# Kernel optimization log

Hardware: AMD Instinct MI355X
Metric: run time of the kernel (lower is better)

The kernel has to match this reference:

```python
import jax, jax.numpy as jnp
import numpy as np

B, T, D, C = 16, 4096, 1024, 128


def setup_inputs() -> dict:
    key = jax.random.key(0)
    ks = jax.random.split(key, 15)

    def w(k, out_dim, in_dim):
        return jax.random.normal(k, (out_dim, in_dim), jnp.float32) / np.sqrt(in_dim).astype(np.float32)

    return {
        "x": jax.random.normal(ks[0], (B, T, D), jnp.float32),
        "Wq": w(ks[1], C, D), "bq": jnp.zeros((C,), jnp.float32),
        "Wk": w(ks[2], C, D), "bk": jnp.zeros((C,), jnp.float32),
        "Wv": w(ks[3], C, D), "bv": jnp.zeros((C,), jnp.float32),
        "Wa": w(ks[4], 1, D), "ba": jnp.zeros((1,), jnp.float32),
        "Wb": w(ks[5], 1, D), "bb": jnp.zeros((1,), jnp.float32),
        "Wg": w(ks[6], C, D), "bg": jnp.zeros((C,), jnp.float32),
        "Wo": w(ks[7], D, C), "bo": jnp.zeros((D,), jnp.float32),
    }


def reference(x, Wq, bq, Wk, bk, Wv, bv, Wa, ba, Wb, bb, Wg, bg, Wo, bo):
    # Projections (torch Linear: y = x @ W.T + b)
    q = x @ Wq.T + bq                                   # (B,T,C)
    k = x @ Wk.T + bk
    k = k / jnp.maximum(jnp.linalg.norm(k, axis=-1, keepdims=True), 1e-12)  # F.normalize
    v = x @ Wv.T + bv
    alpha = jax.nn.sigmoid(x @ Wa.T + ba)               # (B,T,1)
    beta = jax.nn.sigmoid(x @ Wb.T + bb)                # (B,T,1)
    gate = jax.nn.sigmoid(x @ Wg.T + bg)                # (B,T,C)

    Bb, Tt, Dd = x.shape
    Cc = q.shape[-1]

    def step(S, inp):
        q_t, k_t, v_t, a_t, b_t = inp                   # (B,C),(B,C),(B,C),(B,1),(B,1)
        a = a_t[:, :, None]                              # (B,1,1)
        b = b_t[:, :, None]                              # (B,1,1)
        # S @ (a*(I - b*k k^T)) = a*(S - b*(S k) k^T)
        Sk = jnp.einsum('bij,bj->bi', S, k_t)            # (B,C)
        S = a * (S - b * (Sk[:, :, None] * k_t[:, None, :])) \
            + b * (v_t[:, :, None] * k_t[:, None, :])
        o = jnp.einsum('bi,bij->bj', q_t, S)             # (B,C)
        return S, o

    xs = (q.swapaxes(0, 1), k.swapaxes(0, 1), v.swapaxes(0, 1),
          alpha.swapaxes(0, 1), beta.swapaxes(0, 1))     # time-major
    S0 = jnp.zeros((Bb, Cc, Cc), x.dtype)
    _, o = jax.lax.scan(step, S0, xs)                    # o: (T,B,C)
    o = o.swapaxes(0, 1) * gate                          # (B,T,C)
    return o @ Wo.T + bo                                 # (B,T,D)
```

## Files before the change

kernel.cpp:

```cpp
#include <hip/hip_runtime.h>
#include <hip/hip_bf16.h>
#include <math.h>

#define NB 16
#define NT 4096
#define ND 1024
#define NCC 128
#define LCH 64
#define NCHUNK 64
#define BTROWS 65536

typedef __bf16 v8bf __attribute__((ext_vector_type(8)));
typedef float  v4f  __attribute__((ext_vector_type(4)));

static __device__ __forceinline__ float sig_(float x){ return 1.0f/(1.0f + __expf(-x)); }
static __device__ __forceinline__ float dot4_(float4 a, float4 b){
    return a.x*b.x + a.y*b.y + a.z*b.z + a.w*b.w;
}

static __device__ __forceinline__ v8bf pack8(float4 a, float4 b){
    v8bf v;
    v[0]=(__bf16)a.x; v[1]=(__bf16)a.y; v[2]=(__bf16)a.z; v[3]=(__bf16)a.w;
    v[4]=(__bf16)b.x; v[5]=(__bf16)b.y; v[6]=(__bf16)b.z; v[7]=(__bf16)b.w;
    return v;
}

static __device__ __forceinline__ void gload16(const void* g, void* l){
    __builtin_amdgcn_global_load_lds(
        (const __attribute__((address_space(1))) unsigned int*)g,
        (__attribute__((address_space(3))) unsigned int*)l, 16, 0, 0);
}

__global__ __launch_bounds__(256) void k_xcast(
    const float* __restrict__ x, const float* __restrict__ Wa,
    const float* __restrict__ Wb, const float* __restrict__ ba,
    const float* __restrict__ bb2, __bf16* __restrict__ xbf,
    float* __restrict__ ab, float* __restrict__ beb)
{
    const int tid = threadIdx.x;
    const int w = tid >> 6, lane = tid & 63;
    const size_t row = (size_t)blockIdx.x*4 + w;
    const float* xr = x + row*ND + lane*16;
    float4 f0 = ((const float4*)xr)[0];
    float4 f1 = ((const float4*)xr)[1];
    float4 f2 = ((const float4*)xr)[2];
    float4 f3 = ((const float4*)xr)[3];
    const float4* wa = (const float4*)(Wa + lane*16);
    const float4* wb = (const float4*)(Wb + lane*16);
    float da = dot4_(f0,wa[0]) + dot4_(f1,wa[1]) + dot4_(f2,wa[2]) + dot4_(f3,wa[3]);
    float db = dot4_(f0,wb[0]) + dot4_(f1,wb[1]) + dot4_(f2,wb[2]) + dot4_(f3,wb[3]);
    __bf16* xd = xbf + row*ND + lane*16;
    *(v8bf*)(xd)   = pack8(f0,f1);
    *(v8bf*)(xd+8) = pack8(f2,f3);
    #pragma unroll
    for (int m=1;m<64;m<<=1){ da += __shfl_xor(da,m,64); db += __shfl_xor(db,m,64); }
    if (lane == 0){
        ab[row]  = sig_(da + ba[0]);
        beb[row] = sig_(db + bb2[0]);
    }
}

__global__ __launch_bounds__(256) void k_wcast(
    const float* __restrict__ Wq, const float* __restrict__ Wk,
    const float* __restrict__ Wv, const float* __restrict__ Wg,
    __bf16* __restrict__ wbf)
{
    const int tid = threadIdx.x;
    const int w = tid >> 6, lane = tid & 63;
    const int row = blockIdx.x*4 + w;
    const float* src = (row < 128) ? Wq + (size_t)row*ND
                     : (row < 256) ? Wk + (size_t)(row-128)*ND
                     : (row < 384) ? Wv + (size_t)(row-256)*ND
                     :               Wg + (size_t)(row-384)*ND;
    const float4* s4 = (const float4*)(src + lane*16);
    float4 f0=s4[0], f1=s4[1], f2=s4[2], f3=s4[3];
    __bf16* xd = wbf + (size_t)row*ND + lane*16;
    *(v8bf*)(xd)   = pack8(f0,f1);
    *(v8bf*)(xd+8) = pack8(f2,f3);
}

__global__ __launch_bounds__(256) void k_proj2(
    const __bf16* __restrict__ xbf, const __bf16* __restrict__ wbf,
    const float* __restrict__ bq, const float* __restrict__ bk,
    const float* __restrict__ bv, const float* __restrict__ bg,
    float* __restrict__ qb, float* __restrict__ kb2,
    float* __restrict__ vb, float* __restrict__ gb)
{
    __shared__ __attribute__((aligned(16))) __bf16 As[128*64];
    __shared__ __attribute__((aligned(16))) __bf16 Bs[128*64];
    const int tid = threadIdx.x;
    const int lane = tid & 63, w = tid >> 6;
    const int q4 = lane >> 4, l16 = lane & 15;
    const int wm = w >> 1, wn = w & 1;

    const int f = blockIdx.x;
    const int xcd = f & 7, j = f >> 3;
    const int m0 = ((xcd << 6) + (j >> 2)) * 128;
    const int n0 = (j & 3) * 128;

    v4f acc[4][4] = {};

    for (int k0 = 0; k0 < ND; k0 += 64){
        __syncthreads();
        #pragma unroll
        for (int i=0;i<4;i++){
            const int r  = (w*4+i)*8 + (lane >> 3);
            const int ce = (((lane & 7) ^ (r & 7)) << 3);
            gload16(xbf + (size_t)(m0 + r)*ND + k0 + ce, (char*)As + (w*4+i)*1024);
            gload16(wbf + (size_t)(n0 + r)*ND + k0 + ce, (char*)Bs + (w*4+i)*1024);
        }
        __syncthreads();
        #pragma unroll
        for (int ks=0; ks<2; ks++){
            v8bf af[4], bf[4];
            #pragma unroll
            for (int mf=0; mf<4; mf++){
                const int r = wm*64 + mf*16 + l16;
                af[mf] = *(const v8bf*)((const char*)As + r*128 + (((ks*4+q4) ^ (r&7)) << 4));
            }
            #pragma unroll
            for (int nf=0; nf<4; nf++){
                const int r = wn*64 + nf*16 + l16;
                bf[nf] = *(const v8bf*)((const char*)Bs + r*128 + (((ks*4+q4) ^ (r&7)) << 4));
            }
            #pragma unroll
            for (int mf=0; mf<4; mf++)
                #pragma unroll
                for (int nf=0; nf<4; nf++)
                    acc[mf][nf] = __builtin_amdgcn_mfma_f32_16x16x32_bf16(af[mf], bf[nf], acc[mf][nf], 0,0,0);
        }
    }

    #pragma unroll
    for (int mf=0; mf<4; mf++){
        #pragma unroll
        for (int nf=0; nf<4; nf++){
            const int ng  = n0 + wn*64 + nf*16 + l16;
            const int col = ng & 127;
            const int sel = ng >> 7;
            const float bias = (sel==0) ? bq[col] : (sel==1) ? bk[col]
                             : (sel==2) ? bv[col] : bg[col];
            #pragma unroll
            for (int r2=0;r2<4;r2++){
                const int m = m0 + wm*64 + mf*16 + q4*4 + r2;
                const float val = acc[mf][nf][r2] + bias;
                const size_t off = (size_t)m*NCC + col;
                if      (sel == 0) qb[off]  = val;
                else if (sel == 1) kb2[off] = val;
                else if (sel == 2) vb[off]  = val;
                else               gb[off]  = sig_(val);
            }
        }
    }
}

__global__ __launch_bounds__(256) void k_knorm(float* __restrict__ kb){
    const int tid = threadIdx.x;
    const int w = tid >> 6, lane = tid & 63;
    const size_t row = (size_t)blockIdx.x*4 + w;
    float* kr = kb + row*NCC;
    float a = kr[lane], b = kr[lane+64];
    float ss = a*a + b*b;
    #pragma unroll
    for (int m=1;m<64;m<<=1) ss += __shfl_xor(ss, m, 64);
    float inv = 1.0f / fmaxf(sqrtf(ss), 1e-12f);
    kr[lane] = a*inv; kr[lane+64] = b*inv;
}

#define KSWZ(t, j)   ((t)*132 + ((((((j)>>2) ^ ((t)&7))) << 2) | ((j)&3)))
#define KSWZ4(t, j4) ((t)*132 + ((((j4) ^ ((t)&7))) << 2))
#define TSWZ(row, g) ((row)*72 + ((((g) ^ ((row)&7))) << 3))

#define SOLVE_LOOP(RHS_EXPR) \
    _Pragma("unroll") \
    for (int t=0;t<64;t++){ \
        const float* Gr = &Gsh[t*68]; \
        float s0=0.f,s1=0.f,s2=0.f,s3=0.f; \
        _Pragma("unroll") \
        for (int s4=0; s4+4<=t; s4+=4){ \
            float4 g = *(const float4*)(Gr+s4); \
            s0 += g.x*u[s4]; s1 += g.y*u[s4+1]; s2 += g.z*u[s4+2]; s3 += g.w*u[s4+3]; \
        } \
        _Pragma("unroll") \
        for (int s=(t & ~3); s<t; s++) s0 += Gr[s]*u[s]; \
        u[t] = bsh[t]*((RHS_EXPR) - ((s0+s1)+(s2+s3))); \
    }

__global__ __launch_bounds__(256) void k_phaseA(
    const float* __restrict__ kb, float* __restrict__ vb, __bf16* __restrict__ Mb,
    const float* __restrict__ ab, const float* __restrict__ beb,
    float* __restrict__ lgb, __bf16* __restrict__ PTb, float* __restrict__ Rb)
{
    __shared__ __attribute__((aligned(16))) float Ksh[LCH*132];
    __shared__ __attribute__((aligned(16))) float Vsh[LCH*132];
    __shared__ __attribute__((aligned(16))) float Gsh[LCH*68];
    __shared__ __attribute__((aligned(16))) __bf16 KT [NCC*72];
    __shared__ __attribute__((aligned(16))) __bf16 EUT[NCC*72];
    __shared__ __attribute__((aligned(16))) __bf16 EMT[NCC*72];
    __shared__ float lgs[LCH], bsh[LCH], esh[LCH], gam[LCH];

    const int tid = threadIdx.x;
    const int b = blockIdx.x >> 6;
    const int c = blockIdx.x & 63;
    const size_t base = (size_t)b*NT + (size_t)c*LCH;

    if (tid < LCH){
        float la = __logf(fmaxf(ab[base+tid], 1e-30f));
        float ps = la;
        #pragma unroll
        for (int off=1; off<64; off<<=1){
            float o = __shfl_up(ps, off, 64);
            if ((tid & 63) >= off) ps += o;
        }
        lgs[tid] = ps;
        bsh[tid] = beb[base+tid];
    }
    {
        const int row = tid >> 2, seg = tid & 3;
        const float* ks = kb + (base+row)*NCC + seg*32;
        const float* vs = vb + (base+row)*NCC + seg*32;
        #pragma unroll
        for (int i=0;i<32;i+=4){
            float4 kv = *(const float4*)(ks+i);
            float4 vv = *(const float4*)(vs+i);
            *(float4*)(&Ksh[KSWZ4(row, ((seg*32+i)>>2))]) = kv;
            *(float4*)(&Vsh[row*132 + seg*32 + i]) = vv;
        }
    }
    __syncthreads();
    if (tid < LCH){
        lgb[base+tid] = lgs[tid];
        esh[tid] = __expf(lgs[LCH-1] - lgs[tid]);
        gam[tid] = __expf(lgs[tid]);
    }
    for (int idx = tid; idx < (LCH*(LCH+1))/2; idx += 256){
        int t = (int)((sqrtf(8.f*(float)idx + 1.f) - 1.f)*0.5f);
        while ((t+1)*(t+2)/2 <= idx) t++;
        while (t*(t+1)/2 > idx) t--;
        const int s = idx - (t*(t+1))/2;
        float dot = 0.f;
        #pragma unroll 8
        for (int j4=0;j4<32;j4++){
            float4 u = *(const float4*)(&Ksh[KSWZ4(s,j4)]);
            float4 v = *(const float4*)(&Ksh[KSWZ4(t,j4)]);
            dot += u.x*v.x + u.y*v.y + u.z*v.z + u.w*v.w;
        }
        Gsh[t*68+s] = __expf(lgs[t]-lgs[s])*dot;
    }
    {
        const int j = tid & 127, th = tid >> 7;
        #pragma unroll
        for (int g=0; g<4; g++){
            const int t0 = th*32 + g*8;
            v8bf pk;
            #pragma unroll
            for (int e=0;e<8;e++) pk[e] = (__bf16)Ksh[KSWZ(t0+e, j)];
            *(v8bf*)(&KT[TSWZ(j, (t0>>3))]) = pk;
        }
    }
    __syncthreads();

    {
        const int half = tid >> 7, cix = tid & 127;
        float u[64];
        if (half == 0){
            SOLVE_LOOP(Vsh[t*132 + cix])
            #pragma unroll
            for (int t=0;t<64;t++) vb[(base+t)*NCC + cix] = u[t];
            #pragma unroll
            for (int g=0; g<8; g++){
                v8bf pk;
                #pragma unroll
                for (int e=0;e<8;e++) pk[e] = (__bf16)(esh[g*8+e]*u[g*8+e]);
                *(v8bf*)(&EUT[TSWZ(cix, g)]) = pk;
            }
        } else {
            SOLVE_LOOP(gam[t]*Ksh[KSWZ(t, cix)])
            #pragma unroll
            for (int t=0;t<64;t++) Mb[(base+t)*NCC + cix] = (__bf16)u[t];
            #pragma unroll
            for (int g=0; g<8; g++){
                v8bf pk;
                #pragma unroll
                for (int e=0;e<8;e++) pk[e] = (__bf16)(esh[g*8+e]*u[g*8+e]);
                *(v8bf*)(&EMT[TSWZ(cix, g)]) = pk;
            }
        }
    }
    __syncthreads();

    {
        const int lane = tid & 63, w = tid >> 6;
        const int q4 = lane >> 4, l16 = lane & 15;
        const int wm = w >> 1, wn = w & 1;
        const float gl = gam[LCH-1];
        const size_t pbase = ((size_t)(b*NCHUNK + c))*NCC*NCC;
        {
            v4f pacc[4][4] = {};
            #pragma unroll
            for (int ks=0; ks<2; ks++){
                v8bf af[4], bf[4];
                #pragma unroll
                for (int mf=0; mf<4; mf++)
                    af[mf] = *(const v8bf*)(&KT[TSWZ(wm*64+mf*16+l16, ks*4+q4)]);
                #pragma unroll
                for (int nf=0; nf<4; nf++)
                    bf[nf] = *(const v8bf*)(&EMT[TSWZ(wn*64+nf*16+l16, ks*4+q4)]);
                #pragma unroll
                for (int mf=0; mf<4; mf++)
                    #pragma unroll
                    for (int nf=0; nf<4; nf++)
                        pacc[mf][nf] = __builtin_amdgcn_mfma_f32_16x16x32_bf16(af[mf], bf[nf], pacc[mf][nf], 0,0,0);
            }
            #pragma unroll
            for (int mf=0; mf<4; mf++){
                #pragma unroll
                for (int nf=0; nf<4; nf++){
                    const int m = wn*64 + nf*16 + l16;
                    #pragma unroll
                    for (int r=0;r<4;r++){
                        const int j = wm*64 + mf*16 + q4*4 + r;
                        float v = -pacc[mf][nf][r];
                        if (j == m) v += gl;
                        PTb[pbase + (size_t)j*NCC + m] = (__bf16)v;
                    }
                }
            }
        }
        {
            v4f racc[4][4] = {};
            #pragma unroll
            for (int ks=0; ks<2; ks++){
                v8bf af[4], bf[4];
                #pragma unroll
                for (int mf=0; mf<4; mf++)
                    af[mf] = *(const v8bf*)(&EUT[TSWZ(wm*64+mf*16+l16, ks*4+q4)]);
                #pragma unroll
                for (int nf=0; nf<4; nf++)
                    bf[nf] = *(const v8bf*)(&KT[TSWZ(wn*64+nf*16+l16, ks*4+q4)]);
                #pragma unroll
                for (int mf=0; mf<4; mf++)
                    #pragma unroll
                    for (int nf=0; nf<4; nf++)
                        racc[mf][nf] = __builtin_amdgcn_mfma_f32_16x16x32_bf16(af[mf], bf[nf], racc[mf][nf], 0,0,0);
            }
            #pragma unroll
            for (int mf=0; mf<4; mf++){
                #pragma unroll
                for (int nf=0; nf<4; nf++){
                    const int jj = wn*64 + nf*16 + l16;
                    #pragma unroll
                    for (int r=0;r<4;r++){
                        const int i = wm*64 + mf*16 + q4*4 + r;
                        Rb[pbase + (size_t)i*NCC + jj] = racc[mf][nf][r];
                    }
                }
            }
        }
    }
}

__global__ __launch_bounds__(256) void k_phaseB(
    const __bf16* __restrict__ PTb, const float* __restrict__ Rb, float* __restrict__ Sb)
{
    __shared__ __attribute__((aligned(16))) float Ssh[16*132];
    const int tid = threadIdx.x;
    const int b = blockIdx.x >> 3, rb = blockIdx.x & 7;
    const int r0 = rb*16;
    const int lane = tid & 63, w = tid >> 6;
    const int q4 = lane >> 4, l16 = lane & 15;
    for (int i=tid; i<16*132; i+=256) Ssh[i] = 0.f;
    __syncthreads();
    for (int c=0; c<NCHUNK; c++){
        const size_t pbase = ((size_t)(b*NCHUNK + c))*NCC*NCC;
        {
            const int row = tid >> 4, cg = (tid & 15)*8;
            float* dst = Sb + pbase + (size_t)(r0+row)*NCC + cg;
            *(float4*)(dst)   = *(const float4*)(&Ssh[row*132+cg]);
            *(float4*)(dst+4) = *(const float4*)(&Ssh[row*132+cg+4]);
        }
        if (c == NCHUNK-1) break;
        v8bf af[4];
        #pragma unroll
        for (int ks=0; ks<4; ks++){
            const float* sr = &Ssh[l16*132 + ks*32 + q4*8];
            v8bf t;
            #pragma unroll
            for (int j=0;j<8;j++) t[j] = (__bf16)sr[j];
            af[ks] = t;
        }
        __syncthreads();
        v4f acc[2] = {};
        #pragma unroll
        for (int nt=0; nt<2; nt++){
            const int n0 = w*32 + nt*16;
            #pragma unroll
            for (int ks=0; ks<4; ks++){
                v8bf bf = *(const v8bf*)(PTb + pbase + (size_t)(n0+l16)*NCC + ks*32 + q4*8);
                acc[nt] = __builtin_amdgcn_mfma_f32_16x16x32_bf16(af[ks], bf, acc[nt], 0,0,0);
            }
        }
        #pragma unroll
        for (int nt=0; nt<2; nt++){
            const int n = w*32 + nt*16 + l16;
            #pragma unroll
            for (int r=0;r<4;r++){
                const int rowl = q4*4 + r;
                Ssh[rowl*132 + n] = acc[nt][r] + Rb[pbase + (size_t)(r0+rowl)*NCC + n];
            }
        }
        __syncthreads();
    }
}

__global__ __launch_bounds__(256) void k_phaseC(
    const float* __restrict__ qb, const float* __restrict__ kb,
    const float* __restrict__ Ub, const __bf16* __restrict__ Mb,
    const float* __restrict__ Sb, const float* __restrict__ lgb,
    float* __restrict__ gb)
{
    __shared__ __attribute__((aligned(16))) float S0T[NCC*132];
    __shared__ __attribute__((aligned(16))) __bf16 Msh[LCH*136];
    __shared__ __attribute__((aligned(16))) __bf16 Qsh[LCH*136];
    __shared__ __attribute__((aligned(16))) __bf16 Ksh[LCH*136];
    __shared__ __attribute__((aligned(16))) __bf16 Wsh[LCH*136];
    __shared__ __attribute__((aligned(16))) float Ash[LCH*68];
    __shared__ float lgs[LCH];

    const int tid = threadIdx.x;
    const int b = blockIdx.x >> 6, c = blockIdx.x & 63;
    const size_t base = (size_t)b*NT + (size_t)c*LCH;
    const size_t pbase = ((size_t)(b*NCHUNK + c))*NCC*NCC;

    {
        const int i = tid >> 1, j0 = (tid & 1)*64;
        const float* src = Sb + pbase + (size_t)i*NCC + j0;
        #pragma unroll 4
        for (int j=0;j<64;j+=4){
            float4 v = *(const float4*)(src+j);
            S0T[(j0+j  )*132 + i] = v.x;
            S0T[(j0+j+1)*132 + i] = v.y;
            S0T[(j0+j+2)*132 + i] = v.z;
            S0T[(j0+j+3)*132 + i] = v.w;
        }
    }
    {
        const int row = tid >> 2, seg = tid & 3;
        const __bf16* ms = Mb + (base+row)*NCC + seg*32;
        const float* qs = qb + (base+row)*NCC + seg*32;
        const float* ks = kb + (base+row)*NCC + seg*32;
        *(v8bf*)(&Msh[row*136+seg*32])    = *(const v8bf*)(ms);
        *(v8bf*)(&Msh[row*136+seg*32+8])  = *(const v8bf*)(ms+8);
        *(v8bf*)(&Msh[row*136+seg*32+16]) = *(const v8bf*)(ms+16);
        *(v8bf*)(&Msh[row*136+seg*32+24]) = *(const v8bf*)(ms+24);
        #pragma unroll 8
        for (int i=0;i<32;i++){
            Qsh[row*136+seg*32+i] = (__bf16)qs[i];
            Ksh[row*136+seg*32+i] = (__bf16)ks[i];
        }
    }
    if (tid < LCH) lgs[tid] = lgb[base+tid];
    __syncthreads();

    {
        const int tg = tid >> 5, ig = tid & 31;
        float acc[8][4] = {};
        for (int j=0;j<NCC;j++){
            float m8[8];
            #pragma unroll
            for (int r=0;r<8;r++) m8[r] = (float)Msh[(tg*8+r)*136 + j];
            float4 sv = *(const float4*)(&S0T[j*132 + ig*4]);
            #pragma unroll
            for (int r=0;r<8;r++){
                acc[r][0] += m8[r]*sv.x; acc[r][1] += m8[r]*sv.y;
                acc[r][2] += m8[r]*sv.z; acc[r][3] += m8[r]*sv.w;
            }
        }
        #pragma unroll
        for (int r=0;r<8;r++){
            const int t = tg*8+r;
            const float4 uv = *(const float4*)(Ub + (base+t)*NCC + ig*4);
            Wsh[t*136+ig*4+0] = (__bf16)(uv.x - acc[r][0]);
            Wsh[t*136+ig*4+1] = (__bf16)(uv.y - acc[r][1]);
            Wsh[t*136+ig*4+2] = (__bf16)(uv.z - acc[r][2]);
            Wsh[t*136+ig*4+3] = (__bf16)(uv.w - acc[r][3]);
        }
    }
    float o2[8][4];
    {
        const int tg = tid >> 5, jg = tid & 31;
        float acc[8][4] = {};
        for (int i=0;i<NCC;i++){
            float q8[8];
            #pragma unroll
            for (int r=0;r<8;r++) q8[r] = (float)Qsh[(tg*8+r)*136 + i];
            float s4[4];
            #pragma unroll
            for (int rr=0;rr<4;rr++) s4[rr] = S0T[(jg+32*rr)*132 + i];
            #pragma unroll
            for (int r=0;r<8;r++){
                acc[r][0] += q8[r]*s4[0]; acc[r][1] += q8[r]*s4[1];
                acc[r][2] += q8[r]*s4[2]; acc[r][3] += q8[r]*s4[3];
            }
        }
        #pragma unroll
        for (int r=0;r<8;r++){
            const float g = __expf(lgs[tg*8+r]);
            #pragma unroll
            for (int d=0;d<4;d++) o2[r][d] = g*acc[r][d];
        }
    }
    __syncthreads();
    {
        const int tg2 = tid >> 4, sg = tid & 15;
        float acc[4][4] = {};
        for (int i=0;i<NCC;i++){
            float qv[4], wv[4];
            #pragma unroll
            for (int r=0;r<4;r++){
                qv[r] = (float)Qsh[(tg2+16*r)*136 + i];
                wv[r] = (float)Wsh[(sg+16*r)*136 + i];
            }
            #pragma unroll
            for (int a2=0;a2<4;a2++){
                acc[a2][0] += qv[a2]*wv[0]; acc[a2][1] += qv[a2]*wv[1];
                acc[a2][2] += qv[a2]*wv[2]; acc[a2][3] += qv[a2]*wv[3];
            }
        }
        #pragma unroll
        for (int a2=0;a2<4;a2++){
            const int t = tg2 + 16*a2;
            #pragma unroll
            for (int b2=0;b2<4;b2++){
                const int s = sg + 16*b2;
                Ash[t*68+s] = (s <= t) ? __expf(lgs[t]-lgs[s])*acc[a2][b2] : 0.f;
            }
        }
    }
    __syncthreads();
    {
        const int tg = tid >> 5, jg = tid & 31;
        float acc[8][4] = {};
        for (int s=0;s<LCH;s++){
            float a8[8];
            #pragma unroll
            for (int r=0;r<8;r++) a8[r] = Ash[(tg*8+r)*68 + s];
            float k4[4];
            #pragma unroll
            for (int rr=0;rr<4;rr++) k4[rr] = (float)Ksh[s*136 + jg + 32*rr];
            #pragma unroll
            for (int r=0;r<8;r++){
                acc[r][0] += a8[r]*k4[0]; acc[r][1] += a8[r]*k4[1];
                acc[r][2] += a8[r]*k4[2]; acc[r][3] += a8[r]*k4[3];
            }
        }
        #pragma unroll
        for (int r=0;r<8;r++){
            const int t = tg*8+r;
            #pragma unroll
            for (int d=0;d<4;d++){
                const int j = jg + 32*d;
                const size_t off = (base+t)*NCC + j;
                gb[off] = (acc[r][d] + o2[r][d]) * gb[off];
            }
        }
    }
}

__global__ __launch_bounds__(256) void k_out(
    const float* __restrict__ ob, const float* __restrict__ Wo,
    const float* __restrict__ bo, float* __restrict__ out)
{
    __shared__ __attribute__((aligned(16))) __bf16 As[128*40];
    __shared__ __attribute__((aligned(16))) __bf16 Bs[64*40];
    const int tid = threadIdx.x;
    const int m0 = blockIdx.x*128, n0 = blockIdx.y*64;
    const int lane = tid & 63, w = tid >> 6;
    const int q4 = lane >> 4, l16 = lane & 15;
    const int arow = tid >> 1, aseg = tid & 1;
    const int brow = tid >> 2, bseg = tid & 3;
    const float* asrc = ob + (size_t)(m0+arow)*NCC;
    const float* bsrc = Wo + (size_t)(n0+brow)*NCC;

    v4f acc[2][4] = {};

    for (int k0=0; k0<NCC; k0+=32){
        __syncthreads();
        {
            float4 f0 = *(const float4*)(asrc + k0 + aseg*16);
            float4 f1 = *(const float4*)(asrc + k0 + aseg*16 + 4);
            float4 f2 = *(const float4*)(asrc + k0 + aseg*16 + 8);
            float4 f3 = *(const float4*)(asrc + k0 + aseg*16 + 12);
            *(v8bf*)(&As[arow*40 + aseg*16])     = pack8(f0,f1);
            *(v8bf*)(&As[arow*40 + aseg*16 + 8]) = pack8(f2,f3);
        }
        {
            float4 g0 = *(const float4*)(bsrc + k0 + bseg*8);
            float4 g1 = *(const float4*)(bsrc + k0 + bseg*8 + 4);
            *(v8bf*)(&Bs[brow*40 + bseg*8]) = pack8(g0,g1);
        }
        __syncthreads();
        v8bf af0 = *(const v8bf*)(&As[(w*32 + l16)*40 + q4*8]);
        v8bf af1 = *(const v8bf*)(&As[(w*32 + 16 + l16)*40 + q4*8]);
        #pragma unroll
        for (int nt=0; nt<4; nt++){
            v8bf bf = *(const v8bf*)(&Bs[(nt*16 + l16)*40 + q4*8]);
            acc[0][nt] = __builtin_amdgcn_mfma_f32_16x16x32_bf16(af0, bf, acc[0][nt], 0,0,0);
            acc[1][nt] = __builtin_amdgcn_mfma_f32_16x16x32_bf16(af1, bf, acc[1][nt], 0,0,0);
        }
    }
    #pragma unroll
    for (int mt=0; mt<2; mt++){
        #pragma unroll
        for (int nt=0; nt<4; nt++){
            const int n = n0 + nt*16 + l16;
            const float bias = bo[n];
            #pragma unroll
            for (int r=0;r<4;r++){
                const int m = m0 + w*32 + mt*16 + q4*4 + r;
                out[(size_t)m*ND + n] = acc[mt][nt][r] + bias;
            }
        }
    }
}

extern "C" void kernel_launch(void* const* d_in, const int* in_sizes, int n_in,
                              void* d_out, int out_size, void* d_ws, size_t ws_size,
                              hipStream_t stream)
{
    const float* x  = (const float*)d_in[0];
    const float* Wq = (const float*)d_in[1];
    const float* bq = (const float*)d_in[2];
    const float* Wk = (const float*)d_in[3];
    const float* bk = (const float*)d_in[4];
    const float* Wv = (const float*)d_in[5];
    const float* bv = (const float*)d_in[6];
    const float* Wa = (const float*)d_in[7];
    const float* ba = (const float*)d_in[8];
    const float* Wb = (const float*)d_in[9];
    const float* bb2= (const float*)d_in[10];
    const float* Wg = (const float*)d_in[11];
    const float* bg = (const float*)d_in[12];
    const float* Wo = (const float*)d_in[13];
    const float* bo = (const float*)d_in[14];

    char* ws = (char*)d_ws;
    const size_t SZ = (size_t)BTROWS*NCC*4;
    float*  qb  = (float*)(ws + 0*SZ);
    float*  kb  = (float*)(ws + 1*SZ);
    float*  vb  = (float*)(ws + 2*SZ);
    __bf16* Mb  = (__bf16*)(ws + 3*SZ);
    float*  gb  = (float*)(ws + 4*SZ);
    float*  Sb  = (float*)(ws + 5*SZ);
    float*  Rb  = (float*)(ws + 7*SZ);
    __bf16* PTb = (__bf16*)(ws + 9*SZ);
    float*  ab  = (float*)(ws + 10*SZ);
    float*  beb = (float*)(ws + 10*SZ + 262144);
    float*  lgb = (float*)(ws + 10*SZ + 524288);
    __bf16* xbf = (__bf16*)(ws + 5*SZ);
    __bf16* wbf = (__bf16*)(ws + 9*SZ);
    if (ws_size < 10*SZ + 786432) return;

    dim3 blk(256);
    k_wcast <<<dim3(128),            blk, 0, stream>>>(Wq,Wk,Wv,Wg,wbf);
    k_xcast <<<dim3(BTROWS/4),       blk, 0, stream>>>(x,Wa,Wb,ba,bb2,xbf,ab,beb);
    k_proj2 <<<dim3(2048),           blk, 0, stream>>>(xbf,wbf,bq,bk,bv,bg,qb,kb,vb,gb);
    k_knorm <<<dim3(BTROWS/4),       blk, 0, stream>>>(kb);
    k_phaseA<<<dim3(NB*NCHUNK),      blk, 0, stream>>>(kb, vb, Mb, ab, beb, lgb, PTb, Rb);
    k_phaseB<<<dim3(NB*8),           blk, 0, stream>>>(PTb, Rb, Sb);
    k_phaseC<<<dim3(NB*NCHUNK),      blk, 0, stream>>>(qb, kb, vb, Mb, Sb, lgb, gb);
    k_out   <<<dim3(BTROWS/128, 16), blk, 0, stream>>>(gb, Wo, bo, (float*)d_out);
}
```

Baseline: 1.208 ms.

## Rewrite chunk output phase with bf16 MFMA and swizzled LDS layouts

Replaces the four scalar FP32 FMA matmuls in k_phaseC (M·S0, Q·S0, Q·Wᵀ, A·K) with 16x16x32 bf16 MFMA instructions. S0 is staged into LDS in bf16 in both row and transposed forms, K is stored transposed with an XOR swizzle (TSWZ), and the MA buffer is reused for the decay-masked attention matrix. This targets the ALU-bound scalar loops and cuts LDS footprint. It adds more bf16 rounding of S0 and the intermediate attention matrix, and the kernel relies on a TSWZ macro defined outside the shown hunk.

```diff
diff --git a/kernel.cpp b/kernel.cpp
--- a/kernel.cpp
+++ b/kernel.cpp
@@ -419,149 +419,142 @@
     const float* __restrict__ Sb, const float* __restrict__ lgb,
     float* __restrict__ gb)
 {
-    __shared__ __attribute__((aligned(16))) float S0T[NCC*132];
-    __shared__ __attribute__((aligned(16))) __bf16 Msh[LCH*136];
-    __shared__ __attribute__((aligned(16))) __bf16 Qsh[LCH*136];
-    __shared__ __attribute__((aligned(16))) __bf16 Ksh[LCH*136];
+    __shared__ __attribute__((aligned(16))) __bf16 S0r[NCC*136];
+    __shared__ __attribute__((aligned(16))) __bf16 S0t[NCC*136];
+    __shared__ __attribute__((aligned(16))) __bf16 MA [LCH*136];
     __shared__ __attribute__((aligned(16))) __bf16 Wsh[LCH*136];
-    __shared__ __attribute__((aligned(16))) float Ash[LCH*68];
+    __shared__ __attribute__((aligned(16))) __bf16 KT [NCC*72];
     __shared__ float lgs[LCH];
 
     const int tid = threadIdx.x;
     const int b = blockIdx.x >> 6, c = blockIdx.x & 63;
     const size_t base = (size_t)b*NT + (size_t)c*LCH;
     const size_t pbase = ((size_t)(b*NCHUNK + c))*NCC*NCC;
-
-    {
-        const int i = tid >> 1, j0 = (tid & 1)*64;
-        const float* src = Sb + pbase + (size_t)i*NCC + j0;
-        #pragma unroll 4
-        for (int j=0;j<64;j+=4){
-            float4 v = *(const float4*)(src+j);
-            S0T[(j0+j  )*132 + i] = v.x;
-            S0T[(j0+j+1)*132 + i] = v.y;
-            S0T[(j0+j+2)*132 + i] = v.z;
-            S0T[(j0+j+3)*132 + i] = v.w;
-        }
-    }
-    {
-        const int row = tid >> 2, seg = tid & 3;
-        const __bf16* ms = Mb + (base+row)*NCC + seg*32;
-        const float* qs = qb + (base+row)*NCC + seg*32;
-        const float* ks = kb + (base+row)*NCC + seg*32;
-        *(v8bf*)(&Msh[row*136+seg*32])    = *(const v8bf*)(ms);
-        *(v8bf*)(&Msh[row*136+seg*32+8])  = *(const v8bf*)(ms+8);
-        *(v8bf*)(&Msh[row*136+seg*32+16]) = *(const v8bf*)(ms+16);
-        *(v8bf*)(&Msh[row*136+seg*32+24]) = *(const v8bf*)(ms+24);
-        #pragma unroll 8
-        for (int i=0;i<32;i++){
-            Qsh[row*136+seg*32+i] = (__bf16)qs[i];
-            Ksh[row*136+seg*32+i] = (__bf16)ks[i];
-        }
-    }
+    const int lane = tid & 63, w = tid >> 6;
+    const int q4 = lane >> 4, l16 = lane & 15;
+
     if (tid < LCH) lgs[tid] = lgb[base+tid];
+    {
+        const int i = tid >> 1, jh = (tid & 1)*64;
+        const float* src = Sb + pbase + (size_t)i*NCC + jh;
+        #pragma unroll
+        for (int g=0; g<8; g++){
+            float4 a = *(const float4*)(src + g*8);
+            float4 d = *(const float4*)(src + g*8 + 4);
+            v8bf pk = pack8(a,d);
+            *(v8bf*)(&S0r[i*136 + jh + g*8]) = pk;
+            #pragma unroll
+            for (int e=0;e<8;e++) S0t[(jh + g*8 + e)*136 + i] = pk[e];
+        }
+    }
+    {
+        const int row = tid >> 2, seg = (tid & 3)*32;
+        const __bf16* ms = Mb + (base+row)*NCC + seg;
+        *(v8bf*)(&MA[row*136 + seg])      = *(const v8bf*)(ms);
+        *(v8bf*)(&MA[row*136 + seg + 8])  = *(const v8bf*)(ms+8);
+        *(v8bf*)(&MA[row*136 + seg + 16]) = *(const v8bf*)(ms+16);
+        *(v8bf*)(&MA[row*136 + seg + 24]) = *(const v8bf*)(ms+24);
+    }
+    {
+        const int j = tid & 127, th = tid >> 7;
+        #pragma unroll
+        for (int g=0; g<4; g++){
+            const int sg = th*4 + g;
+            const int s0 = sg*8;
+            v8bf pk;
+            #pragma unroll
+            for (int e=0;e<8;e++) pk[e] = (__bf16)kb[(base+s0+e)*NCC + j];
+            *(v8bf*)(&KT[TSWZ(j, sg)]) = pk;
+        }
+    }
+    v8bf qf[4];
+    #pragma unroll
+    for (int ks=0; ks<4; ks++){
+        const float* qs = qb + (base + w*16 + l16)*NCC + ks*32 + q4*8;
+        float4 a = *(const float4*)(qs);
+        float4 d = *(const float4*)(qs+4);
+        qf[ks] = pack8(a,d);
+    }
     __syncthreads();
 
     {
-        const int tg = tid >> 5, ig = tid & 31;
-        float acc[8][4] = {};
-        for (int j=0;j<NCC;j++){
-            float m8[8];
-            #pragma unroll
-            for (int r=0;r<8;r++) m8[r] = (float)Msh[(tg*8+r)*136 + j];
-            float4 sv = *(const float4*)(&S0T[j*132 + ig*4]);
-            #pragma unroll
-            for (int r=0;r<8;r++){
-                acc[r][0] += m8[r]*sv.x; acc[r][1] += m8[r]*sv.y;
-                acc[r][2] += m8[r]*sv.z; acc[r][3] += m8[r]*sv.w;
-            }
-        }
-        #pragma unroll
-        for (int r=0;r<8;r++){
-            const int t = tg*8+r;
-            const float4 uv = *(const float4*)(Ub + (base+t)*NCC + ig*4);
-            Wsh[t*136+ig*4+0] = (__bf16)(uv.x - acc[r][0]);
-            Wsh[t*136+ig*4+1] = (__bf16)(uv.y - acc[r][1]);
-            Wsh[t*136+ig*4+2] = (__bf16)(uv.z - acc[r][2]);
-            Wsh[t*136+ig*4+3] = (__bf16)(uv.w - acc[r][3]);
-        }
-    }
-    float o2[8][4];
-    {
-        const int tg = tid >> 5, jg = tid & 31;
-        float acc[8][4] = {};
-        for (int i=0;i<NCC;i++){
-            float q8[8];
-            #pragma unroll
-            for (int r=0;r<8;r++) q8[r] = (float)Qsh[(tg*8+r)*136 + i];
-            float s4[4];
-            #pragma unroll
-            for (int rr=0;rr<4;rr++) s4[rr] = S0T[(jg+32*rr)*132 + i];
-            #pragma unroll
-            for (int r=0;r<8;r++){
-                acc[r][0] += q8[r]*s4[0]; acc[r][1] += q8[r]*s4[1];
-                acc[r][2] += q8[r]*s4[2]; acc[r][3] += q8[r]*s4[3];
-            }
-        }
-        #pragma unroll
-        for (int r=0;r<8;r++){
-            const float g = __expf(lgs[tg*8+r]);
-            #pragma unroll
-            for (int d=0;d<4;d++) o2[r][d] = g*acc[r][d];
+        v4f x1[8] = {};
+        #pragma unroll
+        for (int ks=0; ks<4; ks++){
+            v8bf af = *(const v8bf*)(&MA[(w*16+l16)*136 + ks*32 + q4*8]);
+            #pragma unroll
+            for (int ib=0; ib<8; ib++){
+                v8bf bf = *(const v8bf*)(&S0r[(ib*16+l16)*136 + ks*32 + q4*8]);
+                x1[ib] = __builtin_amdgcn_mfma_f32_16x16x32_bf16(af, bf, x1[ib], 0,0,0);
+            }
+        }
+        #pragma unroll
+        for (int ib=0; ib<8; ib++){
+            #pragma unroll
+            for (int r=0;r<4;r++){
+                const int t = w*16 + q4*4 + r;
+                const int i = ib*16 + l16;
+                const float u = Ub[(base+t)*NCC + i];
+                Wsh[t*136 + i] = (__bf16)(u - x1[ib][r]);
+            }
+        }
+    }
+    v4f o2[8] = {};
+    #pragma unroll
+    for (int ks=0; ks<4; ks++){
+        #pragma unroll
+        for (int jb=0; jb<8; jb++){
+            v8bf bf = *(const v8bf*)(&S0t[(jb*16+l16)*136 + ks*32 + q4*8]);
+            o2[jb] = __builtin_amdgcn_mfma_f32_16x16x32_bf16(qf[ks], bf, o2[jb], 0,0,0);
         }
     }
     __syncthreads();
-    {
-        const int tg2 = tid >> 4, sg = tid & 15;
-        float acc[4][4] = {};
-        for (int i=0;i<NCC;i++){
-            float qv[4], wv[4];
+
+    {
+        v4f x2[4] = {};
+        #pragma unroll
+        for (int ks=0; ks<4; ks++){
+            #pragma unroll
+            for (int sb=0; sb<4; sb++){
+                v8bf bf = *(const v8bf*)(&Wsh[(sb*16+l16)*136 + ks*32 + q4*8]);
+                x2[sb] = __builtin_amdgcn_mfma_f32_16x16x32_bf16(qf[ks], bf, x2[sb], 0,0,0);
+            }
+        }
+        #pragma unroll
+        for (int sb=0; sb<4; sb++){
             #pragma unroll
             for (int r=0;r<4;r++){
-                qv[r] = (float)Qsh[(tg2+16*r)*136 + i];
-                wv[r] = (float)Wsh[(sg+16*r)*136 + i];
-            }
-            #pragma unroll
-            for (int a2=0;a2<4;a2++){
-                acc[a2][0] += qv[a2]*wv[0]; acc[a2][1] += qv[a2]*wv[1];
-                acc[a2][2] += qv[a2]*wv[2]; acc[a2][3] += qv[a2]*wv[3];
-            }
-        }
-        #pragma unroll
-        for (int a2=0;a2<4;a2++){
-            const int t = tg2 + 16*a2;
-            #pragma unroll
-            for (int b2=0;b2<4;b2++){
-                const int s = sg + 16*b2;
-                Ash[t*68+s] = (s <= t) ? __expf(lgs[t]-lgs[s])*acc[a2][b2] : 0.f;
+                const int t = w*16 + q4*4 + r;
+                const int s = sb*16 + l16;
+                const float v = (s <= t) ? __expf(lgs[t]-lgs[s])*x2[sb][r] : 0.f;
+                MA[t*72 + ((((s>>3) ^ (t&7))) << 3) + (s&7)] = (__bf16)v;
             }
         }
     }
     __syncthreads();
-    {
-        const int tg = tid >> 5, jg = tid & 31;
-        float acc[8][4] = {};
-        for (int s=0;s<LCH;s++){
-            float a8[8];
-            #pragma unroll
-            for (int r=0;r<8;r++) a8[r] = Ash[(tg*8+r)*68 + s];
-            float k4[4];
-            #pragma unroll
-            for (int rr=0;rr<4;rr++) k4[rr] = (float)Ksh[s*136 + jg + 32*rr];
-            #pragma unroll
-            for (int r=0;r<8;r++){
-                acc[r][0] += a8[r]*k4[0]; acc[r][1] += a8[r]*k4[1];
-                acc[r][2] += a8[r]*k4[2]; acc[r][3] += a8[r]*k4[3];
-            }
-        }
-        #pragma unroll
-        for (int r=0;r<8;r++){
-            const int t = tg*8+r;
-            #pragma unroll
-            for (int d=0;d<4;d++){
-                const int j = jg + 32*d;
-                const size_t off = (base+t)*NCC + j;
-                gb[off] = (acc[r][d] + o2[r][d]) * gb[off];
+
+    {
+        v4f o1[8] = {};
+        #pragma unroll
+        for (int ks=0; ks<2; ks++){
+            v8bf af = *(const v8bf*)(&MA[TSWZ(w*16+l16, ks*4+q4)]);
+            #pragma unroll
+            for (int jb=0; jb<8; jb++){
+                v8bf bf = *(const v8bf*)(&KT[TSWZ(jb*16+l16, ks*4+q4)]);
+                o1[jb] = __builtin_amdgcn_mfma_f32_16x16x32_bf16(af, bf, o1[jb], 0,0,0);
+            }
+        }
+        float gam4[4];
+        #pragma unroll
+        for (int r=0;r<4;r++) gam4[r] = __expf(lgs[w*16 + q4*4 + r]);
+        #pragma unroll
+        for (int jb=0; jb<8; jb++){
+            #pragma unroll
+            for (int r=0;r<4;r++){
+                const int t = w*16 + q4*4 + r;
+                const int j = jb*16 + l16;
+                const size_t off = (size_t)(base+t)*NCC + j;
+                gb[off] = (o1[jb][r] + gam4[r]*o2[jb][r]) * gb[off];
             }
         }
     }
```

Result: faster. 1.073 ms (-11.2%).
